# Kernel optimization log

Hardware: AMD Instinct MI355X
Metric: run time of the kernel (lower is better)

Reference implementation:

```python
import jax, jax.numpy as jnp
import numpy as np

B, S, F, D = 2, 576, 16, 512   # batch, spatial tokens (24x24), frames, query_dim
H, C = 8, 64                   # heads, dim_head; inner = H*C = 512


def setup_inputs() -> dict:
    key = jax.random.key(0)
    ks = jax.random.split(key, 6)
    x = jax.random.normal(ks[0], (B, S, F, D), jnp.float32)
    # alternating drop pattern over frames 2..F-1; identical per batch row,
    # as the module requires (it reshapes kept indices to [bs, -1] and takes
    # valid_num from row 0)
    pat = jnp.tile(jnp.array([1, 0], jnp.int64), (F - 2) // 2)
    drop_mask = jnp.broadcast_to(pat, (B, F - 2))
    sd = 1.0 / np.sqrt(D)
    Wq = jax.random.normal(ks[1], (D, H * C), jnp.float32) * sd
    Wk = jax.random.normal(ks[2], (D, H * C), jnp.float32) * sd
    Wv = jax.random.normal(ks[3], (D, H * C), jnp.float32) * sd
    Wout = jax.random.normal(ks[4], (H * C, D), jnp.float32) * (1.0 / np.sqrt(H * C))
    bout = jnp.zeros((D,), jnp.float32)
    return {"x": x, "drop_mask": drop_mask, "Wq": Wq, "Wk": Wk, "Wv": Wv,
            "Wout": Wout, "bout": bout}


def _sdpa(q, k, v):
    # q: [..., Lq, C], k/v: [..., Lk, C]; xformers default scale = 1/sqrt(C)
    scale = 1.0 / np.sqrt(q.shape[-1])
    logits = jnp.einsum('...qc,...kc->...qk', q, k) * scale
    w = jax.nn.softmax(logits, axis=-1)
    return jnp.einsum('...qk,...kc->...qc', w, v)


def reference(x, drop_mask, Wq, Wk, Wv, Wout, bout):
    b, s, f, _ = x.shape
    h, c = H, C
    q = x @ Wq  # [b, s, f, h*c]
    k = x @ Wk
    v = x @ Wv

    # ---- per-frame spatial self-attention for frames 1: ('b s f (h c) -> (b f h) s c')
    def to_bfhsc(t, nf):
        return t.reshape(b, s, nf, h, c).transpose(0, 2, 3, 1, 4)  # b f h s c

    ress = _sdpa(to_bfhsc(q[:, :, 1:], f - 1),
                 to_bfhsc(k[:, :, 1:], f - 1),
                 to_bfhsc(v[:, :, 1:], f - 1))            # [b, f-1, h, s, c]
    ress = ress.transpose(0, 3, 1, 2, 4).reshape(b, s, f - 1, h * c)

    # ---- frame-0 temporal attention over first 2 frames + non-dropped frames
    dm = np.asarray(drop_mask)
    valid = int((f - 2) - dm[0].sum())
    # kept frame indices (into frames 2..f-1), per batch row
    kept = np.stack([np.nonzero(dm[i] == 0)[0] for i in range(b)])  # [b, valid]
    idx = jnp.asarray(kept)[:, None, :, None]
    ka, va = k[:, :, 2:], v[:, :, 2:]                     # [b, s, f-2, h*c]
    ki = jnp.take_along_axis(ka, jnp.broadcast_to(idx, (b, s, valid, h * c)), axis=2)
    vi = jnp.take_along_axis(va, jnp.broadcast_to(idx, (b, s, valid, h * c)), axis=2)
    dk = jnp.concatenate([k[:, :, :2], ki], axis=2)        # [b, s, df, h*c]
    dv = jnp.concatenate([v[:, :, :2], vi], axis=2)
    df = 2 + valid

    qt = q[:, :, 0].reshape(b, s, h, c).transpose(0, 2, 1, 3)  # [b, h, s, c]
    kt = dk.reshape(b, s, df, h, c).transpose(0, 3, 1, 2, 4).reshape(b, h, s * df, c)
    vt = dv.reshape(b, s, df, h, c).transpose(0, 3, 1, 2, 4).reshape(b, h, s * df, c)
    resq = _sdpa(qt, kt, vt)                               # [b, h, s, c]
    resq = resq.transpose(0, 2, 1, 3).reshape(b, s, 1, h * c)

    res = jnp.concatenate([resq, ress], axis=2)            # [b, s, f, h*c]
    return res @ Wout + bout                               # [b, s, f, D]
```

## Files before the change

kernel.cpp:

```cpp
#include <hip/hip_runtime.h>
#include <math.h>

#define Bb 2
#define Ss 576
#define Ff 16
#define Hh 8
#define Cc 64
#define HC 512
#define Mrows (Bb * Ss * Ff)

typedef __bf16 bf16x8 __attribute__((ext_vector_type(8)));
typedef float  f32x4  __attribute__((ext_vector_type(4)));
typedef float  f32x16 __attribute__((ext_vector_type(16)));
typedef unsigned short u16;
typedef unsigned int   u32;

#if __has_builtin(__builtin_amdgcn_exp2f)
#define EXP2(x) __builtin_amdgcn_exp2f(x)
#else
#define EXP2(x) exp2f(x)
#endif

#define QSCALE 0.18033688011112042f

__device__ __forceinline__ u16 f2bf(float f) {
    union { __bf16 b; u16 u; } cv;
    cv.b = (__bf16)f;
    return cv.u;
}

__device__ __forceinline__ f32x16 zero16() {
    f32x16 z;
#pragma unroll
    for (int i = 0; i < 16; ++i) z[i] = 0.f;
    return z;
}

__device__ __forceinline__ int swz8(int row, int g) {
    return row * 64 + (((g ^ (row & 7) ^ (((row >> 3) & 1) << 1)) & 7) << 3);
}

__device__ __forceinline__ uint4 pack8(float4 a, float4 b) {
    union { u16 s[8]; uint4 v; } u;
    u.s[0] = f2bf(a.x); u.s[1] = f2bf(a.y); u.s[2] = f2bf(a.z); u.s[3] = f2bf(a.w);
    u.s[4] = f2bf(b.x); u.s[5] = f2bf(b.y); u.s[6] = f2bf(b.z); u.s[7] = f2bf(b.w);
    return u.v;
}

__device__ __forceinline__ void gl_lds16(const u16* g, u16* l) {
    __builtin_amdgcn_global_load_lds(
        (const __attribute__((address_space(1))) u32*)g,
        (__attribute__((address_space(3))) u32*)l, 16, 0, 0);
}

__global__ __launch_bounds__(256) void prep_kernel(
    const float* __restrict__ W0, const float* __restrict__ W1,
    const float* __restrict__ W2, const float* __restrict__ W3,
    const float* __restrict__ x,
    u16* __restrict__ Wt, u16* __restrict__ xb)
{
    __shared__ float Ts[64][65];
    const int mz = blockIdx.z;
    const int t = threadIdx.x;
    if (mz >= 4) {
        int id = (mz - 4) * 64 + blockIdx.y * 8 + blockIdx.x;
        size_t i = ((size_t)id * 256 + t) * 8;
        float4 a = *(const float4*)&x[i];
        float4 b = *(const float4*)&x[i + 4];
        *(uint4*)&xb[i] = pack8(a, b);
        return;
    }
    const float* W = (mz == 0) ? W0 : (mz == 1) ? W1 : (mz == 2) ? W2 : W3;
    u16* Wo = Wt + (size_t)mz * 512 * 512;
    const int k0 = blockIdx.x * 64, n0 = blockIdx.y * 64;
#pragma unroll
    for (int p = 0; p < 4; ++p) {
        int idx = t + p * 256;
        int row = idx >> 4, cg = idx & 15;
        *(float4*)&Ts[row][cg * 4] =
            *(const float4*)&W[(size_t)(k0 + row) * 512 + n0 + cg * 4];
    }
    __syncthreads();
#pragma unroll
    for (int p = 0; p < 2; ++p) {
        int idx = t + p * 256;
        int row = idx >> 3, cg = idx & 7;
        union { u16 s[8]; uint4 v; } u;
#pragma unroll
        for (int j = 0; j < 8; ++j) u.s[j] = f2bf(Ts[cg * 8 + j][row]);
        *(uint4*)&Wo[(size_t)(n0 + row) * 512 + k0 + cg * 8] = u.v;
    }
}

__global__ __launch_bounds__(256) void qkv_kernel(
    const u16* __restrict__ xb, const u16* __restrict__ Wt,
    u16* __restrict__ q, u16* __restrict__ k, u16* __restrict__ vT)
{
    __shared__ u16 As[128 * 32];
    __shared__ u16 Bs[128 * 32];
    const int bi = blockIdx.x;
    const int mt = bi % 144;
    const int mm = bi / 144;
    const int nt = mm & 3, mat = mm >> 2;
    const int t = threadIdx.x;
    const int w = t >> 6, L = t & 63;
    const int m0 = mt * 128, n0 = nt * 128;
    const int wm = (w >> 1) * 64, wn = (w & 1) * 64;

    const int srow = t >> 2, scg = t & 3;
    const int ma0 = m0 + srow, ma1 = ma0 + 64;
    const int b0 = ma0 / 9216, r0 = ma0 % 9216, f0 = r0 / 576, s0 = r0 % 576;
    const int b1 = ma1 / 9216, r1 = ma1 % 9216, f1 = r1 / 576, s1 = r1 % 576;
    const u16* xp0 = xb + ((size_t)(b0 * 576 + s0) * 16 + f0) * 512 + scg * 8;
    const u16* xp1 = xb + ((size_t)(b1 * 576 + s1) * 16 + f1) * 512 + scg * 8;
    const u16* Bp = Wt + (size_t)mat * 512 * 512 + (size_t)(n0 + srow) * 512 + scg * 8;

    f32x4 acc[4][4];
#pragma unroll
    for (int i = 0; i < 4; ++i)
#pragma unroll
        for (int j = 0; j < 4; ++j) acc[i][j] = (f32x4){0.f, 0.f, 0.f, 0.f};

    for (int k0 = 0; k0 < 512; k0 += 32) {
        __syncthreads();
        gl_lds16(xp0 + k0, &As[t * 8]);
        gl_lds16(xp1 + k0, &As[2048 + t * 8]);
        gl_lds16(Bp + k0, &Bs[t * 8]);
        gl_lds16(Bp + k0 + 64 * 512, &Bs[2048 + t * 8]);
        __syncthreads();
        bf16x8 af[4], bfr[4];
#pragma unroll
        for (int i = 0; i < 4; ++i) {
            af[i]  = *(const bf16x8*)&As[(wm + 16 * i + (L & 15)) * 32 + (L >> 4) * 8];
            bfr[i] = *(const bf16x8*)&Bs[(wn + 16 * i + (L & 15)) * 32 + (L >> 4) * 8];
        }
#pragma unroll
        for (int i = 0; i < 4; ++i)
#pragma unroll
            for (int j = 0; j < 4; ++j)
                acc[i][j] = __builtin_amdgcn_mfma_f32_16x16x32_bf16(
                    af[i], bfr[j], acc[i][j], 0, 0, 0);
    }

    if (mat < 2) {
        u16* Cout = (mat == 0) ? q : k;
        const float scale = (mat == 0) ? QSCALE : 1.0f;
#pragma unroll
        for (int i = 0; i < 4; ++i)
#pragma unroll
            for (int j = 0; j < 4; ++j)
#pragma unroll
                for (int r = 0; r < 4; ++r) {
                    int row = m0 + wm + 16 * i + (L >> 4) * 4 + r;
                    int col = n0 + wn + 16 * j + (L & 15);
                    float vv = acc[i][j][r] * scale;
                    float pvv = __shfl_xor(vv, 1);
                    if (!(L & 1)) {
                        u32 pk2 = (u32)f2bf(vv) | ((u32)f2bf(pvv) << 16);
                        *(u32*)(Cout + (size_t)row * 512 + col) = pk2;
                    }
                }
    } else {
#pragma unroll
        for (int i = 0; i < 4; ++i) {
            int row = m0 + wm + 16 * i + (L >> 4) * 4;
            int bb = row / 9216, rr = row % 9216;
            int f = rr / 576, s = rr % 576;
#pragma unroll
            for (int j = 0; j < 4; ++j) {
                int col = n0 + wn + 16 * j + (L & 15);
                int h = col >> 6, c = col & 63;
                union { u16 s4[4]; uint2 v; } u;
#pragma unroll
                for (int r = 0; r < 4; ++r) u.s4[r] = f2bf(acc[i][j][r]);
                *(uint2*)&vT[((((size_t)(bb * 16 + f) * 8 + h) * 64 + c) * 576) + s] = u.v;
            }
        }
    }
}

__global__ __launch_bounds__(256) void gemm_out_kernel(
    const u16* __restrict__ res, const u16* __restrict__ Wt3,
    const float* __restrict__ bout, float* __restrict__ out)
{
    __shared__ u16 As[128 * 32];
    __shared__ u16 Bs[128 * 32];
    const int bi = blockIdx.x;
    const int mt = bi % 144, nt = bi / 144;
    const int t = threadIdx.x;
    const int w = t >> 6, L = t & 63;
    const int m0 = mt * 128, n0 = nt * 128;
    const int wm = (w >> 1) * 64, wn = (w & 1) * 64;

    const int srow = t >> 2, scg = t & 3;
    const u16* Ap = res + (size_t)(m0 + srow) * 512 + scg * 8;
    const u16* Bp = Wt3 + (size_t)(n0 + srow) * 512 + scg * 8;

    f32x4 acc[4][4];
#pragma unroll
    for (int i = 0; i < 4; ++i)
#pragma unroll
        for (int j = 0; j < 4; ++j) acc[i][j] = (f32x4){0.f, 0.f, 0.f, 0.f};

    for (int k0 = 0; k0 < 512; k0 += 32) {
        __syncthreads();
        gl_lds16(Ap + k0, &As[t * 8]);
        gl_lds16(Ap + k0 + 64 * 512, &As[2048 + t * 8]);
        gl_lds16(Bp + k0, &Bs[t * 8]);
        gl_lds16(Bp + k0 + 64 * 512, &Bs[2048 + t * 8]);
        __syncthreads();
        bf16x8 af[4], bfr[4];
#pragma unroll
        for (int i = 0; i < 4; ++i) {
            af[i]  = *(const bf16x8*)&As[(wm + 16 * i + (L & 15)) * 32 + (L >> 4) * 8];
            bfr[i] = *(const bf16x8*)&Bs[(wn + 16 * i + (L & 15)) * 32 + (L >> 4) * 8];
        }
#pragma unroll
        for (int i = 0; i < 4; ++i)
#pragma unroll
            for (int j = 0; j < 4; ++j)
                acc[i][j] = __builtin_amdgcn_mfma_f32_16x16x32_bf16(
                    af[i], bfr[j], acc[i][j], 0, 0, 0);
    }

#pragma unroll
    for (int i = 0; i < 4; ++i)
#pragma unroll
        for (int r = 0; r < 4; ++r) {
            int row = m0 + wm + 16 * i + (L >> 4) * 4 + r;
            int bb = row / 9216, rr = row % 9216;
            int f = rr / 576, s = rr % 576;
            size_t obase = ((size_t)(bb * 576 + s) * 16 + f) * 512;
#pragma unroll
            for (int j = 0; j < 4; ++j) {
                int col = n0 + wn + 16 * j + (L & 15);
                out[obase + col] = acc[i][j][r] + bout[col];
            }
        }
}

__global__ __launch_bounds__(256, 4) void attn_kernel(
    const u16* __restrict__ q, const u16* __restrict__ k,
    const u16* __restrict__ vT, const int* __restrict__ dm,
    u16* __restrict__ res, float* __restrict__ po, float* __restrict__ pl)
{
    __shared__ u16 Ks[64 * 64];
    __shared__ u16 Vts[64 * 64];

    const int t = threadIdx.x;
    const int w = t >> 6, L = t & 63;
    const int half = L >> 5, l31 = L & 31;
    const int bi = blockIdx.x;

    int b, h, qt, qframe, fi, mode;
    if (bi < 720) {
        mode = 0;
        qt = bi / 144;
        int g = bi % 144;
        int bh = g / 9; fi = g % 9;
        b = bh >> 3; h = bh & 7; qframe = 0;
    } else {
        mode = 1;
        int u = bi - 720;
        int g = u % 240;
        qt = u / 240;
        b = g / 120;
        int rr = g % 120;
        qframe = 1 + (rr >> 3); h = rr & 7; fi = 0;
    }

    int kf;
    if (mode == 1) {
        kf = qframe;
    } else if (fi < 2) {
        kf = fi;
    } else {
        int n = 2; kf = 2;
#pragma unroll
        for (int j = 0; j < Ff - 2; ++j) {
            if (dm[b * (Ff - 2) + j] == 0) { if (n == fi) kf = 2 + j; ++n; }
        }
    }

    const int q0 = qt * 128;
    const bool active = (q0 + 32 * w) < Ss;
    const int qrow = q0 + 32 * w + l31;

    bf16x8 qf[4];
    if (active) {
        const u16* qp = q + ((size_t)(b * 16 + qframe) * Ss + qrow) * 512 + h * 64 + 8 * half;
#pragma unroll
        for (int ks = 0; ks < 4; ++ks) qf[ks] = *(const bf16x8*)(qp + 16 * ks);
    }

    float lsum = 0.f;
    f32x16 o[2] = {zero16(), zero16()};

    const int srow = t >> 2, sc2 = (t & 3) * 2;
    const int lk0 = swz8(srow, sc2), lk1 = swz8(srow, sc2 + 1);
    const u16* kbase = k + ((size_t)(b * 16 + kf) * Ss) * 512 + h * 64;
    const u16* vbase = vT + (((size_t)(b * 16 + kf) * 8 + h) * 64) * (size_t)Ss;

    uint4 ka, kb2, va, vb2;
    {
        const u16* kp = kbase + (size_t)srow * 512 + sc2 * 8;
        ka  = *(const uint4*)kp;
        kb2 = *(const uint4*)(kp + 8);
        const u16* vp = vbase + (size_t)srow * Ss + sc2 * 8;
        va  = *(const uint4*)vp;
        vb2 = *(const uint4*)(vp + 8);
    }

    for (int kt = 0; kt < 9; ++kt) {
        __syncthreads();
        *(uint4*)&Ks[lk0]  = ka;
        *(uint4*)&Ks[lk1]  = kb2;
        *(uint4*)&Vts[lk0] = va;
        *(uint4*)&Vts[lk1] = vb2;
        __syncthreads();

        if (kt < 8) {
            int s0 = (kt + 1) * 64;
            const u16* kp = kbase + (size_t)(s0 + srow) * 512 + sc2 * 8;
            ka  = *(const uint4*)kp;
            kb2 = *(const uint4*)(kp + 8);
            const u16* vp = vbase + (size_t)srow * Ss + s0 + sc2 * 8;
            va  = *(const uint4*)vp;
            vb2 = *(const uint4*)(vp + 8);
        }

        if (active) {
#pragma unroll
            for (int hb = 0; hb < 2; ++hb) {
                f32x16 st = zero16();
#pragma unroll
                for (int ks = 0; ks < 4; ++ks) {
                    bf16x8 a = *(const bf16x8*)&Ks[swz8(32 * hb + l31, 2 * ks + half)];
                    st = __builtin_amdgcn_mfma_f32_32x32x16_bf16(a, qf[ks], st, 0, 0, 0);
                }
#pragma unroll
                for (int kk = 0; kk < 2; ++kk) {
                    const int ks = 2 * hb + kk;
                    float e0 = EXP2(st[8 * kk + 0]), e1 = EXP2(st[8 * kk + 1]);
                    float e2 = EXP2(st[8 * kk + 2]), e3 = EXP2(st[8 * kk + 3]);
                    float e4 = EXP2(st[8 * kk + 4]), e5 = EXP2(st[8 * kk + 5]);
                    float e6 = EXP2(st[8 * kk + 6]), e7 = EXP2(st[8 * kk + 7]);
                    lsum += ((e0 + e1) + (e2 + e3)) + ((e4 + e5) + (e6 + e7));
                    u32 x0 = (u32)f2bf(e0) | ((u32)f2bf(e1) << 16);
                    u32 z0 = (u32)f2bf(e2) | ((u32)f2bf(e3) << 16);
                    u32 x1 = (u32)f2bf(e4) | ((u32)f2bf(e5) << 16);
                    u32 z1 = (u32)f2bf(e6) | ((u32)f2bf(e7) << 16);
                    auto sx = __builtin_amdgcn_permlane32_swap(x0, x1, false, false);
                    auto sz = __builtin_amdgcn_permlane32_swap(z0, z1, false, false);
                    union { u32 u[4]; bf16x8 v; } pu;
                    pu.u[0] = sx[0]; pu.u[1] = sz[0]; pu.u[2] = sx[1]; pu.u[3] = sz[1];
                    bf16x8 v0 = *(const bf16x8*)&Vts[swz8(l31,      2 * ks + half)];
                    bf16x8 v1 = *(const bf16x8*)&Vts[swz8(32 + l31, 2 * ks + half)];
                    o[0] = __builtin_amdgcn_mfma_f32_32x32x16_bf16(v0, pu.v, o[0], 0, 0, 0);
                    o[1] = __builtin_amdgcn_mfma_f32_32x32x16_bf16(v1, pu.v, o[1], 0, 0, 0);
                }
            }
        }
    }

    if (!active) return;
    lsum += __shfl_xor(lsum, 32);

    if (mode == 1) {
        float inv = 1.f / lsum;
        u16* rp = res + ((size_t)(b * 16 + qframe) * Ss + qrow) * 512 + h * 64;
#pragma unroll
        for (int cg = 0; cg < 2; ++cg)
#pragma unroll
            for (int g = 0; g < 4; ++g) {
                union { u16 s4[4]; uint2 v; } u;
#pragma unroll
                for (int r = 0; r < 4; ++r) u.s4[r] = f2bf(o[cg][4 * g + r] * inv);
                *(uint2*)&rp[32 * cg + 8 * g + 4 * half] = u.v;
            }
    } else {
        int bh = b * 8 + h;
        float* pp = po + ((size_t)(fi * 16 + bh) * Ss + qrow) * 64;
#pragma unroll
        for (int cg = 0; cg < 2; ++cg)
#pragma unroll
            for (int g = 0; g < 4; ++g) {
                float4 v4 = make_float4(o[cg][4 * g + 0], o[cg][4 * g + 1],
                                        o[cg][4 * g + 2], o[cg][4 * g + 3]);
                *(float4*)&pp[32 * cg + 8 * g + 4 * half] = v4;
            }
        if (half == 0) pl[(size_t)(fi * 16 + bh) * Ss + qrow] = lsum;
    }
}

__global__ __launch_bounds__(256) void merge_kernel(
    const float* __restrict__ po, const float* __restrict__ pl,
    u16* __restrict__ res)
{
    int tid = blockIdx.x * 256 + threadIdx.x;
    int c4 = tid & 15;
    int rem = tid >> 4;
    int qg = rem % Ss;
    int bh = rem / Ss;
    int b = bh >> 3, h = bh & 7;
    float4 acc = make_float4(0.f, 0.f, 0.f, 0.f);
    float ls = 0.f;
#pragma unroll
    for (int fi = 0; fi < 9; ++fi) {
        const float4 v = *(const float4*)&po[((size_t)(fi * 16 + bh) * Ss + qg) * 64 + c4 * 4];
        acc.x += v.x; acc.y += v.y; acc.z += v.z; acc.w += v.w;
        ls += pl[(size_t)(fi * 16 + bh) * Ss + qg];
    }
    float inv = 1.f / ls;
    union { u16 s4[4]; uint2 v; } u;
    u.s4[0] = f2bf(acc.x * inv); u.s4[1] = f2bf(acc.y * inv);
    u.s4[2] = f2bf(acc.z * inv); u.s4[3] = f2bf(acc.w * inv);
    *(uint2*)&res[((size_t)(b * 16 + 0) * Ss + qg) * 512 + h * 64 + c4 * 4] = u.v;
}

extern "C" void kernel_launch(void* const* d_in, const int* in_sizes, int n_in,
                              void* d_out, int out_size, void* d_ws, size_t ws_size,
                              hipStream_t stream)
{
    (void)in_sizes; (void)n_in; (void)out_size; (void)ws_size;
    const float* x    = (const float*)d_in[0];
    const int*   dmsk = (const int*)  d_in[1];
    const float* Wq   = (const float*)d_in[2];
    const float* Wk   = (const float*)d_in[3];
    const float* Wv   = (const float*)d_in[4];
    const float* Wout = (const float*)d_in[5];
    const float* bout = (const float*)d_in[6];
    float* out = (float*)d_out;

    const size_t NE = (size_t)Mrows * HC;
    u16* q   = (u16*)d_ws;
    u16* kk  = q   + NE;
    u16* vT  = kk  + NE;
    u16* res = vT  + NE;
    u16* Wt  = res + NE;
    float* po = (float*)(Wt + (size_t)4 * 512 * 512);
    float* pl = po + (size_t)9 * 16 * Ss * 64;
    u16* xb = res;

    prep_kernel<<<dim3(8, 8, 76), 256, 0, stream>>>(Wq, Wk, Wv, Wout, x, Wt, xb);
    qkv_kernel<<<1728, 256, 0, stream>>>(xb, Wt, q, kk, vT);
    attn_kernel<<<1920, 256, 0, stream>>>(q, kk, vT, dmsk, res, po, pl);
    merge_kernel<<<576, 256, 0, stream>>>(po, pl, res);
    gemm_out_kernel<<<576, 256, 0, stream>>>(
        res, Wt + (size_t)3 * 512 * 512, bout, out);
}
```

Before: 218.5 us.

## Fuse frame-0 split-KV merge into attention via last-block atomic counter

Drops the separate merge kernel. Each frame-0 attention block now bumps a per-(query tile, batch-head) counter after writing its partial output and softmax sum, and the ninth block to arrive reduces all partials and writes the bf16 result. The counters are zeroed inside the prep kernel. This saves one kernel launch and its gap, at the cost of threadfences, an atomic, and a serialized tail reduction in the last-arriving block.

Result: slower. 395.5 us (+81.0%).

```diff
diff --git a/kernel.cpp b/kernel.cpp
--- a/kernel.cpp
+++ b/kernel.cpp
@@ -57,12 +57,13 @@
     const float* __restrict__ W0, const float* __restrict__ W1,
     const float* __restrict__ W2, const float* __restrict__ W3,
     const float* __restrict__ x,
-    u16* __restrict__ Wt, u16* __restrict__ xb)
+    u16* __restrict__ Wt, u16* __restrict__ xb, int* __restrict__ cnt)
 {
     __shared__ float Ts[64][65];
     const int mz = blockIdx.z;
     const int t = threadIdx.x;
     if (mz >= 4) {
+        if (mz == 4 && blockIdx.x == 0 && blockIdx.y == 0 && t < 80) cnt[t] = 0;
         int id = (mz - 4) * 64 + blockIdx.y * 8 + blockIdx.x;
         size_t i = ((size_t)id * 256 + t) * 8;
         float4 a = *(const float4*)&x[i];
@@ -242,10 +243,12 @@
 __global__ __launch_bounds__(256, 4) void attn_kernel(
     const u16* __restrict__ q, const u16* __restrict__ k,
     const u16* __restrict__ vT, const int* __restrict__ dm,
-    u16* __restrict__ res, float* __restrict__ po, float* __restrict__ pl)
+    u16* __restrict__ res, float* __restrict__ po, float* __restrict__ pl,
+    int* __restrict__ cnt)
 {
     __shared__ u16 Ks[64 * 64];
     __shared__ u16 Vts[64 * 64];
+    __shared__ int sflag;
 
     const int t = threadIdx.x;
     const int w = t >> 6, L = t & 63;
@@ -363,10 +366,9 @@
         }
     }
 
-    if (!active) return;
-    lsum += __shfl_xor(lsum, 32);
-
     if (mode == 1) {
+        if (!active) return;
+        lsum += __shfl_xor(lsum, 32);
         float inv = 1.f / lsum;
         u16* rp = res + ((size_t)(b * 16 + qframe) * Ss + qrow) * 512 + h * 64;
 #pragma unroll
@@ -378,9 +380,13 @@
                 for (int r = 0; r < 4; ++r) u.s4[r] = f2bf(o[cg][4 * g + r] * inv);
                 *(uint2*)&rp[32 * cg + 8 * g + 4 * half] = u.v;
             }
-    } else {
-        int bh = b * 8 + h;
-        float* pp = po + ((size_t)(fi * 16 + bh) * Ss + qrow) * 64;
+        return;
+    }
+
+    const int bh2 = b * 8 + h;
+    if (active) {
+        lsum += __shfl_xor(lsum, 32);
+        float* pp = po + ((size_t)(fi * 16 + bh2) * Ss + qrow) * 64;
 #pragma unroll
         for (int cg = 0; cg < 2; ++cg)
 #pragma unroll
@@ -389,33 +395,37 @@
                                         o[cg][4 * g + 2], o[cg][4 * g + 3]);
                 *(float4*)&pp[32 * cg + 8 * g + 4 * half] = v4;
             }
-        if (half == 0) pl[(size_t)(fi * 16 + bh) * Ss + qrow] = lsum;
-    }
-}
-
-__global__ __launch_bounds__(256) void merge_kernel(
-    const float* __restrict__ po, const float* __restrict__ pl,
-    u16* __restrict__ res)
-{
-    int tid = blockIdx.x * 256 + threadIdx.x;
-    int c4 = tid & 15;
-    int rem = tid >> 4;
-    int qg = rem % Ss;
-    int bh = rem / Ss;
-    int b = bh >> 3, h = bh & 7;
-    float4 acc = make_float4(0.f, 0.f, 0.f, 0.f);
-    float ls = 0.f;
-#pragma unroll
-    for (int fi = 0; fi < 9; ++fi) {
-        const float4 v = *(const float4*)&po[((size_t)(fi * 16 + bh) * Ss + qg) * 64 + c4 * 4];
-        acc.x += v.x; acc.y += v.y; acc.z += v.z; acc.w += v.w;
-        ls += pl[(size_t)(fi * 16 + bh) * Ss + qg];
-    }
-    float inv = 1.f / ls;
-    union { u16 s4[4]; uint2 v; } u;
-    u.s4[0] = f2bf(acc.x * inv); u.s4[1] = f2bf(acc.y * inv);
-    u.s4[2] = f2bf(acc.z * inv); u.s4[3] = f2bf(acc.w * inv);
-    *(uint2*)&res[((size_t)(b * 16 + 0) * Ss + qg) * 512 + h * 64 + c4 * 4] = u.v;
+        if (half == 0) pl[(size_t)(fi * 16 + bh2) * Ss + qrow] = lsum;
+    }
+
+    __threadfence();
+    __syncthreads();
+    if (t == 0) sflag = atomicAdd(&cnt[qt * 16 + bh2], 1);
+    __syncthreads();
+    if (sflag != 8) return;
+
+    __threadfence();
+    const int c4 = t & 15;
+    const int rloc = t >> 4;
+#pragma unroll
+    for (int p = 0; p < 8; ++p) {
+        int qg = q0 + p * 16 + rloc;
+        if (qg < Ss) {
+            float4 acc2 = make_float4(0.f, 0.f, 0.f, 0.f);
+            float ls = 0.f;
+#pragma unroll
+            for (int f2 = 0; f2 < 9; ++f2) {
+                const float4 v = *(const float4*)&po[((size_t)(f2 * 16 + bh2) * Ss + qg) * 64 + c4 * 4];
+                acc2.x += v.x; acc2.y += v.y; acc2.z += v.z; acc2.w += v.w;
+                ls += pl[(size_t)(f2 * 16 + bh2) * Ss + qg];
+            }
+            float inv = 1.f / ls;
+            union { u16 s4[4]; uint2 v; } u;
+            u.s4[0] = f2bf(acc2.x * inv); u.s4[1] = f2bf(acc2.y * inv);
+            u.s4[2] = f2bf(acc2.z * inv); u.s4[3] = f2bf(acc2.w * inv);
+            *(uint2*)&res[((size_t)(b * 16 + 0) * Ss + qg) * 512 + h * 64 + c4 * 4] = u.v;
+        }
+    }
 }
 
 extern "C" void kernel_launch(void* const* d_in, const int* in_sizes, int n_in,
@@ -440,12 +450,12 @@
     u16* Wt  = res + NE;
     float* po = (float*)(Wt + (size_t)4 * 512 * 512);
     float* pl = po + (size_t)9 * 16 * Ss * 64;
+    int* cnt = (int*)(pl + (size_t)9 * 16 * Ss);
     u16* xb = res;
 
-    prep_kernel<<<dim3(8, 8, 76), 256, 0, stream>>>(Wq, Wk, Wv, Wout, x, Wt, xb);
+    prep_kernel<<<dim3(8, 8, 76), 256, 0, stream>>>(Wq, Wk, Wv, Wout, x, Wt, xb, cnt);
     qkv_kernel<<<1728, 256, 0, stream>>>(xb, Wt, q, kk, vT);
-    attn_kernel<<<1920, 256, 0, stream>>>(q, kk, vT, dmsk, res, po, pl);
-    merge_kernel<<<576, 256, 0, stream>>>(po, pl, res);
+    attn_kernel<<<1920, 256, 0, stream>>>(q, kk, vT, dmsk, res, po, pl, cnt);
     gemm_out_kernel<<<576, 256, 0, stream>>>(
         res, Wt + (size_t)3 * 512 * 512, bout, out);
 }
```

## Double-buffer LDS tiles in QKV and output GEMMs to overlap loads with MFMA

Applied to the files above, without the earlier changes.

Both projection GEMM kernels now keep two LDS buffers for the A and B tiles. The global-to-LDS copy of the next K slice is issued before the MFMA work on the current slice, and the loop is unrolled by two so each step needs one barrier instead of two. The aim is to hide global load latency behind compute and cut synchronisation overhead. LDS use per block doubles to 32 KB, which may reduce the number of blocks resident per CU.

New measurement: 235.8 us. 7.9% more time.

```diff
diff --git a/kernel.cpp b/kernel.cpp
--- a/kernel.cpp
+++ b/kernel.cpp
@@ -92,12 +92,30 @@
     }
 }
 
+#define GEMM_STEP(Ab, Bb_)                                                     \
+    {                                                                          \
+        bf16x8 af[4], bfr[4];                                                  \
+        _Pragma("unroll")                                                      \
+        for (int i = 0; i < 4; ++i) {                                          \
+            af[i]  = *(const bf16x8*)&Ab[(wm + 16 * i + (L & 15)) * 32 + (L >> 4) * 8];  \
+            bfr[i] = *(const bf16x8*)&Bb_[(wn + 16 * i + (L & 15)) * 32 + (L >> 4) * 8]; \
+        }                                                                      \
+        _Pragma("unroll")                                                      \
+        for (int i = 0; i < 4; ++i)                                            \
+            _Pragma("unroll")                                                  \
+            for (int j = 0; j < 4; ++j)                                        \
+                acc[i][j] = __builtin_amdgcn_mfma_f32_16x16x32_bf16(           \
+                    af[i], bfr[j], acc[i][j], 0, 0, 0);                        \
+    }
+
 __global__ __launch_bounds__(256) void qkv_kernel(
     const u16* __restrict__ xb, const u16* __restrict__ Wt,
     u16* __restrict__ q, u16* __restrict__ k, u16* __restrict__ vT)
 {
-    __shared__ u16 As[128 * 32];
-    __shared__ u16 Bs[128 * 32];
+    __shared__ u16 As0[128 * 32];
+    __shared__ u16 As1[128 * 32];
+    __shared__ u16 Bs0[128 * 32];
+    __shared__ u16 Bs1[128 * 32];
     const int bi = blockIdx.x;
     const int mt = bi % 144;
     const int mm = bi / 144;
@@ -106,6 +124,7 @@
     const int w = t >> 6, L = t & 63;
     const int m0 = mt * 128, n0 = nt * 128;
     const int wm = (w >> 1) * 64, wn = (w & 1) * 64;
+    const int t8 = t * 8;
 
     const int srow = t >> 2, scg = t & 3;
     const int ma0 = m0 + srow, ma1 = ma0 + 64;
@@ -121,25 +140,29 @@
 #pragma unroll
         for (int j = 0; j < 4; ++j) acc[i][j] = (f32x4){0.f, 0.f, 0.f, 0.f};
 
-    for (int k0 = 0; k0 < 512; k0 += 32) {
-        __syncthreads();
-        gl_lds16(xp0 + k0, &As[t * 8]);
-        gl_lds16(xp1 + k0, &As[2048 + t * 8]);
-        gl_lds16(Bp + k0, &Bs[t * 8]);
-        gl_lds16(Bp + k0 + 64 * 512, &Bs[2048 + t * 8]);
-        __syncthreads();
-        bf16x8 af[4], bfr[4];
-#pragma unroll
-        for (int i = 0; i < 4; ++i) {
-            af[i]  = *(const bf16x8*)&As[(wm + 16 * i + (L & 15)) * 32 + (L >> 4) * 8];
-            bfr[i] = *(const bf16x8*)&Bs[(wn + 16 * i + (L & 15)) * 32 + (L >> 4) * 8];
-        }
-#pragma unroll
-        for (int i = 0; i < 4; ++i)
-#pragma unroll
-            for (int j = 0; j < 4; ++j)
-                acc[i][j] = __builtin_amdgcn_mfma_f32_16x16x32_bf16(
-                    af[i], bfr[j], acc[i][j], 0, 0, 0);
+    gl_lds16(xp0, &As0[t8]);
+    gl_lds16(xp1, &As0[2048 + t8]);
+    gl_lds16(Bp,  &Bs0[t8]);
+    gl_lds16(Bp + 64 * 512, &Bs0[2048 + t8]);
+    __syncthreads();
+
+    for (int it = 0; it < 8; ++it) {
+        const int kB = it * 64 + 32;
+        gl_lds16(xp0 + kB, &As1[t8]);
+        gl_lds16(xp1 + kB, &As1[2048 + t8]);
+        gl_lds16(Bp + kB,  &Bs1[t8]);
+        gl_lds16(Bp + kB + 64 * 512, &Bs1[2048 + t8]);
+        GEMM_STEP(As0, Bs0);
+        __syncthreads();
+        if (it < 7) {
+            const int kN = kB + 32;
+            gl_lds16(xp0 + kN, &As0[t8]);
+            gl_lds16(xp1 + kN, &As0[2048 + t8]);
+            gl_lds16(Bp + kN,  &Bs0[t8]);
+            gl_lds16(Bp + kN + 64 * 512, &Bs0[2048 + t8]);
+        }
+        GEMM_STEP(As1, Bs1);
+        __syncthreads();
     }
 
     if (mat < 2) {
@@ -183,14 +206,17 @@
     const u16* __restrict__ res, const u16* __restrict__ Wt3,
     const float* __restrict__ bout, float* __restrict__ out)
 {
-    __shared__ u16 As[128 * 32];
-    __shared__ u16 Bs[128 * 32];
+    __shared__ u16 As0[128 * 32];
+    __shared__ u16 As1[128 * 32];
+    __shared__ u16 Bs0[128 * 32];
+    __shared__ u16 Bs1[128 * 32];
     const int bi = blockIdx.x;
     const int mt = bi % 144, nt = bi / 144;
     const int t = threadIdx.x;
     const int w = t >> 6, L = t & 63;
     const int m0 = mt * 128, n0 = nt * 128;
     const int wm = (w >> 1) * 64, wn = (w & 1) * 64;
+    const int t8 = t * 8;
 
     const int srow = t >> 2, scg = t & 3;
     const u16* Ap = res + (size_t)(m0 + srow) * 512 + scg * 8;
@@ -202,25 +228,29 @@
 #pragma unroll
         for (int j = 0; j < 4; ++j) acc[i][j] = (f32x4){0.f, 0.f, 0.f, 0.f};
 
-    for (int k0 = 0; k0 < 512; k0 += 32) {
-        __syncthreads();
-        gl_lds16(Ap + k0, &As[t * 8]);
-        gl_lds16(Ap + k0 + 64 * 512, &As[2048 + t * 8]);
-        gl_lds16(Bp + k0, &Bs[t * 8]);
-        gl_lds16(Bp + k0 + 64 * 512, &Bs[2048 + t * 8]);
-        __syncthreads();
-        bf16x8 af[4], bfr[4];
-#pragma unroll
-        for (int i = 0; i < 4; ++i) {
-            af[i]  = *(const bf16x8*)&As[(wm + 16 * i + (L & 15)) * 32 + (L >> 4) * 8];
-            bfr[i] = *(const bf16x8*)&Bs[(wn + 16 * i + (L & 15)) * 32 + (L >> 4) * 8];
-        }
-#pragma unroll
-        for (int i = 0; i < 4; ++i)
-#pragma unroll
-            for (int j = 0; j < 4; ++j)
-                acc[i][j] = __builtin_amdgcn_mfma_f32_16x16x32_bf16(
-                    af[i], bfr[j], acc[i][j], 0, 0, 0);
+    gl_lds16(Ap, &As0[t8]);
+    gl_lds16(Ap + 64 * 512, &As0[2048 + t8]);
+    gl_lds16(Bp, &Bs0[t8]);
+    gl_lds16(Bp + 64 * 512, &Bs0[2048 + t8]);
+    __syncthreads();
+
+    for (int it = 0; it < 8; ++it) {
+        const int kB = it * 64 + 32;
+        gl_lds16(Ap + kB, &As1[t8]);
+        gl_lds16(Ap + kB + 64 * 512, &As1[2048 + t8]);
+        gl_lds16(Bp + kB, &Bs1[t8]);
+        gl_lds16(Bp + kB + 64 * 512, &Bs1[2048 + t8]);
+        GEMM_STEP(As0, Bs0);
+        __syncthreads();
+        if (it < 7) {
+            const int kN = kB + 32;
+            gl_lds16(Ap + kN, &As0[t8]);
+            gl_lds16(Ap + kN + 64 * 512, &As0[2048 + t8]);
+            gl_lds16(Bp + kN, &Bs0[t8]);
+            gl_lds16(Bp + kN + 64 * 512, &Bs0[2048 + t8]);
+        }
+        GEMM_STEP(As1, Bs1);
+        __syncthreads();
     }
 
 #pragma unroll
```
